# Kernel tuning notes

Measured on AMD Instinct MI355X. Metric: run time of the kernel, lower is better.

## Reference

```python
import jax, jax.numpy as jnp
import numpy as np
import math

FACTOR = 5


def setup_inputs() -> dict:
    key = jax.random.key(0)
    k1, k2, k3, k4 = jax.random.split(key, 4)
    B, L, H, D = 8, 1024, 8, 64
    S = FACTOR * math.ceil(math.log(L))  # U_part = 35
    return {
        "queries": jax.random.normal(k1, (B, L, H, D), jnp.float32),
        "keys": jax.random.normal(k2, (B, L, H, D), jnp.float32),
        "values": jax.random.normal(k3, (B, L, H, D), jnp.float32),
        "sample_idx": jax.random.randint(k4, (L, S), 0, L, dtype=jnp.int32),
        "attn_mask": 0,  # unused by the original forward
    }


def reference(queries, keys, values, sample_idx, attn_mask):
    B, L_Q, H, D = queries.shape
    L_K = keys.shape[1]
    # [B, L, H, D] -> [B, H, L, D]
    Q = jnp.transpose(queries, (0, 2, 1, 3))
    K = jnp.transpose(keys, (0, 2, 1, 3))
    V = jnpp_transpose(values) if False else jnp.transpose(values, (0, 2, 1, 3))

    u = min(FACTOR * math.ceil(math.log(L_Q)), L_Q)  # n_top

    # --- _prob_QK: sampled scores, sparsity measure, top-u query selection ---
    K_sample = K[:, :, sample_idx, :]  # [B, H, L_Q, S, D]
    QK_sample = jnp.einsum('bhqd,bhqsd->bhqs', Q, K_sample)  # [B, H, L_Q, S]
    M = QK_sample.max(axis=-1) - QK_sample.sum(axis=-1) / L_K  # [B, H, L_Q]
    _, M_top = jax.lax.top_k(M, u)  # [B, H, u]

    Q_reduce = jnp.take_along_axis(Q, M_top[..., None], axis=2)  # [B, H, u, D]
    scale = 1.0 / math.sqrt(D)
    scores_top = jnp.einsum('bhud,bhkd->bhuk', Q_reduce, K) * scale  # [B, H, u, L_K]

    # --- initial context (mask_flag=True): running causal mean of V ---
    denom = jnp.arange(1, L_K + 1, dtype=V.dtype)[:, None]  # [L_K, 1]
    context = jnp.cumsum(V, axis=2) / denom  # [B, H, L_K, D]

    # --- softmax over keys, sparse update of selected query rows ---
    attn = jax.nn.softmax(scores_top, axis=-1)  # [B, H, u, L_K]
    update = jnp.einsum('bhuk,bhkd->bhud', attn, V)  # [B, H, u, D]

    b_idx = jnp.arange(B)[:, None, None]
    h_idx = jnp.arange(H)[None, :, None]
    context = context.at[b_idx, h_idx, M_top].set(update)

    return jnp.transpose(context, (0, 2, 1, 3))  # [B, L_Q, H, D]
```

## Files before the change

kernel.cpp:

```cpp
#include <hip/hip_runtime.h>
#include <math.h>

#define BB 8
#define LL 1024
#define HH 8
#define DD 64
#define SS 35
#define UU 35
#define BH (BB*HH)
#define NCHK 4
#define CHK 256
#define RPAD 48

#define CSBLOCKS BH
#define MBLOCKS (BB*LL)

typedef __attribute__((ext_vector_type(8))) short short8;
typedef __attribute__((ext_vector_type(4))) float f32x4;

__device__ __forceinline__ size_t qkv_off(int b, int l, int h, int d) {
    return (((size_t)b*LL + l)*HH + h)*DD + d;
}

__device__ __forceinline__ unsigned short f2bf(float x) {
    unsigned int u = __float_as_uint(x);
    u = (u + 0x7fffu + ((u >> 16) & 1u)) >> 16;
    return (unsigned short)u;
}

__device__ __forceinline__ short8 ld_bf8_g(const float* __restrict__ p) {
    float4 x = *reinterpret_cast<const float4*>(p);
    float4 y = *reinterpret_cast<const float4*>(p + 4);
    short8 r;
    r[0] = (short)f2bf(x.x); r[1] = (short)f2bf(x.y);
    r[2] = (short)f2bf(x.z); r[3] = (short)f2bf(x.w);
    r[4] = (short)f2bf(y.x); r[5] = (short)f2bf(y.y);
    r[6] = (short)f2bf(y.z); r[7] = (short)f2bf(y.w);
    return r;
}

__device__ __forceinline__ float red8_shr(float p) {
    int t;
    t = __builtin_amdgcn_update_dpp(0, __float_as_int(p), 0x111, 0xF, 0xF, true);
    p += __int_as_float(t);
    t = __builtin_amdgcn_update_dpp(0, __float_as_int(p), 0x112, 0xF, 0xF, true);
    p += __int_as_float(t);
    t = __builtin_amdgcn_update_dpp(0, __float_as_int(p), 0x114, 0xF, 0xF, true);
    p += __int_as_float(t);
    return p;
}

__global__ __launch_bounds__(512, 2) void kernel_M_cumsum(const float* __restrict__ Q,
                                                          const float* __restrict__ K,
                                                          const float* __restrict__ V,
                                                          const int*   __restrict__ sidx,
                                                          float* __restrict__ M,
                                                          float* __restrict__ out) {
    int blk = blockIdx.x;
    if (blk < CSBLOCKS) {
        __shared__ float partial[8][64];
        int bh = blk;
        int b = bh >> 3, h = bh & 7;
        int d = threadIdx.x & 63, seg = threadIdx.x >> 6;
        int l0 = seg * 128;
        const float* vp = V + qkv_off(b, l0, h, d);

        float s = 0.f;
#pragma unroll 8
        for (int i = 0; i < 128; i++) s += vp[(size_t)i * (HH * DD)];
        partial[seg][d] = s;
        __syncthreads();
        float run = 0.f;
#pragma unroll
        for (int ss = 0; ss < 7; ss++) {
            float v = partial[ss][d];
            run += (ss < seg) ? v : 0.f;
        }
        float* op = out + qkv_off(b, l0, h, d);
#pragma unroll 8
        for (int i = 0; i < 128; i++) {
            run += vp[(size_t)i * (HH * DD)];
            op[(size_t)i * (HH * DD)] = run / (float)(l0 + i + 1);
        }
    } else {
        __shared__ float s_mx[8][8];
        __shared__ float s_sm[8][8];
        int mblk = blk - CSBLOCKS;
        int b = mblk & 7;
        int q = mblk >> 3;
        int tid = threadIdx.x;
        int w = tid >> 6, lane = tid & 63;
        int h = lane >> 3, j = lane & 7, dsub = j * 4;

        const float* qb = Q + ((size_t)(b * LL + q) * HH + h) * DD + dsub;
        f32x4 q0 = *reinterpret_cast<const f32x4*>(qb);
        f32x4 q1 = *reinterpret_cast<const f32x4*>(qb + 32);

        const int* sq = sidx + q * SS;
        int sl[5];
#pragma unroll
        for (int i = 0; i < 5; i++) {
            int s = w + 8 * i;
            sl[i] = sq[s < SS ? s : 0];
        }

        const float* kbase = K + (size_t)b * (LL * HH * DD) + h * DD + dsub;
        f32x4 ka[5], kc[5];
#pragma unroll
        for (int i = 0; i < 5; i++) {
            const float* kp = kbase + (size_t)sl[i] * (HH * DD);
            ka[i] = *reinterpret_cast<const f32x4*>(kp);
            kc[i] = *reinterpret_cast<const f32x4*>(kp + 32);
        }

        float mx = -INFINITY, sm = 0.f;
#pragma unroll
        for (int i = 0; i < 5; i++) {
            float d = q0.x * ka[i].x + q0.y * ka[i].y + q0.z * ka[i].z + q0.w * ka[i].w
                    + q1.x * kc[i].x + q1.y * kc[i].y + q1.z * kc[i].z + q1.w * kc[i].w;
            d = red8_shr(d);
            bool valid = (i < 4) || (w < 3);
            if (valid) { mx = fmaxf(mx, d); sm += d; }
        }
        if (j == 7) { s_mx[w][h] = mx; s_sm[w][h] = sm; }
        __syncthreads();
        if (tid < 8) {
            float m2 = -INFINITY, s2 = 0.f;
#pragma unroll
            for (int ww = 0; ww < 8; ww++) {
                m2 = fmaxf(m2, s_mx[ww][tid]);
                s2 += s_sm[ww][tid];
            }
            M[(b * HH + tid) * LL + q] = m2 - s2 * (1.0f / LL);
        }
    }
}

__global__ __launch_bounds__(64, 4) void kernel_topk(const float* __restrict__ M,
                                                     int* __restrict__ top) {
    int bh = blockIdx.x, lane = threadIdx.x;
    float v[16];
#pragma unroll
    for (int i = 0; i < 16; i++) v[i] = M[bh * LL + i * 64 + lane];

    for (int k = 0; k < UU; k++) {
        float bv = -INFINITY; int bi = 0x7fffffff;
#pragma unroll
        for (int i = 0; i < 16; i++) {
            if (v[i] > bv) { bv = v[i]; bi = i * 64 + lane; }
        }
#pragma unroll
        for (int w = 1; w < 64; w <<= 1) {
            float ov = __shfl_xor(bv, w);
            int   oi = __shfl_xor(bi, w);
            if (ov > bv || (ov == bv && oi < bi)) { bv = ov; bi = oi; }
        }
        if (lane == 0) top[bh * UU + k] = bi;
        if ((bi & 63) == lane) {
            int slot = bi >> 6;
#pragma unroll
            for (int i = 0; i < 16; i++) if (i == slot) v[i] = -INFINITY;
        }
    }
}

__global__ __launch_bounds__(256) void kernel_attn_part(const float* __restrict__ Q,
                                                        const float* __restrict__ K,
                                                        const float* __restrict__ V,
                                                        const int*   __restrict__ top,
                                                        float* __restrict__ m_ws,
                                                        float* __restrict__ se_ws,
                                                        float* __restrict__ pv_ws) {
    __shared__ unsigned short vt[64 * CHK];
    __shared__ unsigned short p_lds[RPAD * CHK];
    __shared__ float red_m[4][RPAD];
    __shared__ float red_se[4][RPAD];
    __shared__ int   qpos_s[RPAD];

    const int blk = blockIdx.x;
    const int bh  = blk >> 2;
    const int ch  = blk & 3;
    const int b   = bh >> 3, h = bh & 7;
    const int l0  = ch * CHK;
    const int tid = threadIdx.x;
    const int w    = tid >> 6;
    const int lane = tid & 63;
    const int c    = lane & 15;
    const int g    = lane >> 4;
    const float scale = 0.125f;

    if (tid < RPAD) qpos_s[tid] = top[bh * UU + (tid < UU ? tid : UU - 1)];

#pragma unroll
    for (int i = 0; i < 8; i++) {
        int task = i * 256 + tid;
        int d   = task & 63;
        int lq8 = task >> 6;
        float vv[8];
#pragma unroll
        for (int j = 0; j < 8; j++)
            vv[j] = V[qkv_off(b, l0 + lq8 * 8 + j, h, d)];
        short8 pk;
#pragma unroll
        for (int j = 0; j < 8; j++) pk[j] = (short)f2bf(vv[j]);
        *reinterpret_cast<short8*>(vt + d * CHK + (((lq8 ^ (d & 31)) << 3))) = pk;
    }
    __syncthreads();

    f32x4 acc[3][4];
#pragma unroll
    for (int mt = 0; mt < 3; mt++)
#pragma unroll
        for (int nt = 0; nt < 4; nt++) acc[mt][nt] = (f32x4){0.f, 0.f, 0.f, 0.f};

#pragma unroll
    for (int ks = 0; ks < 2; ks++) {
        int k0 = ks * 32 + g * 8;
        short8 af[3];
#pragma unroll
        for (int mt = 0; mt < 3; mt++) {
            int row = mt * 16 + c;
            af[mt] = ld_bf8_g(Q + qkv_off(b, qpos_s[row], h, k0));
        }
#pragma unroll
        for (int nt = 0; nt < 4; nt++) {
            int kl = l0 + w * 64 + nt * 16 + c;
            short8 bf = ld_bf8_g(K + qkv_off(b, kl, h, k0));
#pragma unroll
            for (int mt = 0; mt < 3; mt++)
                acc[mt][nt] = __builtin_amdgcn_mfma_f32_16x16x32_bf16(af[mt], bf, acc[mt][nt], 0, 0, 0);
        }
    }

    float tmax[3][4];
#pragma unroll
    for (int mt = 0; mt < 3; mt++)
#pragma unroll
        for (int r = 0; r < 4; r++) {
            float m = fmaxf(fmaxf(acc[mt][0][r], acc[mt][1][r]),
                            fmaxf(acc[mt][2][r], acc[mt][3][r]));
            m = fmaxf(m, __shfl_xor(m, 1));
            m = fmaxf(m, __shfl_xor(m, 2));
            m = fmaxf(m, __shfl_xor(m, 4));
            m = fmaxf(m, __shfl_xor(m, 8));
            tmax[mt][r] = m;
        }
    if (c == 0) {
#pragma unroll
        for (int mt = 0; mt < 3; mt++)
#pragma unroll
            for (int r = 0; r < 4; r++)
                red_m[w][mt * 16 + g * 4 + r] = tmax[mt][r];
    }
    __syncthreads();

    float tse[3][4];
#pragma unroll
    for (int mt = 0; mt < 3; mt++)
#pragma unroll
        for (int r = 0; r < 4; r++) {
            int row = mt * 16 + g * 4 + r;
            float m = fmaxf(fmaxf(red_m[0][row], red_m[1][row]),
                            fmaxf(red_m[2][row], red_m[3][row]));
            float s = 0.f;
#pragma unroll
            for (int nt = 0; nt < 4; nt++) {
                float p = __expf(scale * (acc[mt][nt][r] - m));
                acc[mt][nt][r] = p;
                s += p;
                p_lds[row * CHK + w * 64 + nt * 16 + c] = f2bf(p);
            }
            s += __shfl_xor(s, 1);
            s += __shfl_xor(s, 2);
            s += __shfl_xor(s, 4);
            s += __shfl_xor(s, 8);
            tse[mt][r] = s;
        }
    if (c == 0) {
#pragma unroll
        for (int mt = 0; mt < 3; mt++)
#pragma unroll
            for (int r = 0; r < 4; r++)
                red_se[w][mt * 16 + g * 4 + r] = tse[mt][r];
    }
    __syncthreads();

    if (tid < RPAD) {
        float mm = fmaxf(fmaxf(red_m[0][tid], red_m[1][tid]),
                         fmaxf(red_m[2][tid], red_m[3][tid]));
        float ss = red_se[0][tid] + red_se[1][tid] + red_se[2][tid] + red_se[3][tid];
        m_ws[blk * RPAD + tid]  = mm;
        se_ws[blk * RPAD + tid] = ss;
    }

    f32x4 acc2[3];
#pragma unroll
    for (int mt = 0; mt < 3; mt++) acc2[mt] = (f32x4){0.f, 0.f, 0.f, 0.f};

#pragma unroll
    for (int ks = 0; ks < 8; ks++) {
        int slot = ks * 4 + g;
        int d    = w * 16 + c;
        short8 bf = *reinterpret_cast<const short8*>(
            vt + d * CHK + ((slot ^ (d & 31)) << 3));
#pragma unroll
        for (int mt = 0; mt < 3; mt++) {
            short8 af = *reinterpret_cast<const short8*>(
                p_lds + (mt * 16 + c) * CHK + ks * 32 + g * 8);
            acc2[mt] = __builtin_amdgcn_mfma_f32_16x16x32_bf16(af, bf, acc2[mt], 0, 0, 0);
        }
    }

#pragma unroll
    for (int mt = 0; mt < 3; mt++)
#pragma unroll
        for (int r = 0; r < 4; r++) {
            int row = mt * 16 + g * 4 + r;
            pv_ws[((size_t)blk * RPAD + row) * 64 + w * 16 + c] = acc2[mt][r];
        }
}

__global__ __launch_bounds__(256) void kernel_attn_comb(const int* __restrict__ top,
                                                        const float* __restrict__ m_ws,
                                                        const float* __restrict__ se_ws,
                                                        const float* __restrict__ pv_ws,
                                                        float* __restrict__ out) {
    int bh = blockIdx.x;
    int b = bh >> 3, h = bh & 7;
    const float scale = 0.125f;
    for (int idx = threadIdx.x; idx < UU * 64; idx += 256) {
        int r = idx >> 6, d = idx & 63;
        float mc[NCHK];
        float mm = -INFINITY;
#pragma unroll
        for (int ch = 0; ch < NCHK; ch++) {
            mc[ch] = m_ws[(bh * NCHK + ch) * RPAD + r];
            mm = fmaxf(mm, mc[ch]);
        }
        float num = 0.f, den = 0.f;
#pragma unroll
        for (int ch = 0; ch < NCHK; ch++) {
            float f = __expf(scale * (mc[ch] - mm));
            num += f * pv_ws[((size_t)(bh * NCHK + ch) * RPAD + r) * 64 + d];
            den += f * se_ws[(bh * NCHK + ch) * RPAD + r];
        }
        out[qkv_off(b, top[bh * UU + r], h, d)] = num / den;
    }
}

extern "C" void kernel_launch(void* const* d_in, const int* in_sizes, int n_in,
                              void* d_out, int out_size, void* d_ws, size_t ws_size,
                              hipStream_t stream) {
    const float* Q    = (const float*)d_in[0];
    const float* K    = (const float*)d_in[1];
    const float* V    = (const float*)d_in[2];
    const int*   sidx = (const int*)d_in[3];
    float* out = (float*)d_out;

    char* ws = (char*)d_ws;
    float* M     = (float*)(ws);
    int*   top   = (int*)  (ws + 262144);
    float* m_ws  = (float*)(ws + 272384);
    float* se_ws = (float*)(ws + 321536);
    float* pv_ws = (float*)(ws + 370688);

    kernel_M_cumsum <<<CSBLOCKS + MBLOCKS, 512, 0, stream>>>(Q, K, V, sidx, M, out);
    kernel_topk     <<<BH, 64, 0, stream>>>(M, top);
    kernel_attn_part<<<BH * NCHK, 256, 0, stream>>>(Q, K, V, top, m_ws, se_ws, pv_ws);
    kernel_attn_comb<<<BH, 256, 0, stream>>>(top, m_ws, se_ws, pv_ws, out);
}
```

Before: 81.59 us.

## Stage sampled K rows via global_load_lds, halve block size, speed topk reduction

```diff
diff --git a/kernel.cpp b/kernel.cpp
--- a/kernel.cpp
+++ b/kernel.cpp
@@ -39,6 +39,12 @@
     return r;
 }
 
+__device__ __forceinline__ void gload_lds16(const void* g, void* l) {
+    __builtin_amdgcn_global_load_lds(
+        (const __attribute__((address_space(1))) void*)g,
+        (__attribute__((address_space(3))) void*)l, 16, 0, 0);
+}
+
 __device__ __forceinline__ float red8_shr(float p) {
     int t;
     t = __builtin_amdgcn_update_dpp(0, __float_as_int(p), 0x111, 0xF, 0xF, true);
@@ -50,7 +56,34 @@
     return p;
 }
 
-__global__ __launch_bounds__(512, 2) void kernel_M_cumsum(const float* __restrict__ Q,
+__device__ __forceinline__ float wave_fmax64(float x) {
+    int t;
+    t = __builtin_amdgcn_update_dpp(0, __float_as_int(x), 0xB1, 0xF, 0xF, true);
+    x = fmaxf(x, __int_as_float(t));
+    t = __builtin_amdgcn_update_dpp(0, __float_as_int(x), 0x4E, 0xF, 0xF, true);
+    x = fmaxf(x, __int_as_float(t));
+    t = __builtin_amdgcn_update_dpp(0, __float_as_int(x), 0x141, 0xF, 0xF, true);
+    x = fmaxf(x, __int_as_float(t));
+    t = __builtin_amdgcn_update_dpp(0, __float_as_int(x), 0x140, 0xF, 0xF, true);
+    x = fmaxf(x, __int_as_float(t));
+    x = fmaxf(x, __shfl_xor(x, 16));
+    x = fmaxf(x, __shfl_xor(x, 32));
+    return x;
+}
+
+__device__ __forceinline__ int wave_imin64(int x) {
+    int t;
+    t = __builtin_amdgcn_update_dpp(0, x, 0xB1, 0xF, 0xF, true);  x = (t < x) ? t : x;
+    t = __builtin_amdgcn_update_dpp(0, x, 0x4E, 0xF, 0xF, true);  x = (t < x) ? t : x;
+    t = __builtin_amdgcn_update_dpp(0, x, 0x141, 0xF, 0xF, true); x = (t < x) ? t : x;
+    t = __builtin_amdgcn_update_dpp(0, x, 0x140, 0xF, 0xF, true); x = (t < x) ? t : x;
+    int y;
+    y = __shfl_xor(x, 16); x = (y < x) ? y : x;
+    y = __shfl_xor(x, 32); x = (y < x) ? y : x;
+    return x;
+}
+
+__global__ __launch_bounds__(256, 3) void kernel_M_cumsum(const float* __restrict__ Q,
                                                           const float* __restrict__ K,
                                                           const float* __restrict__ V,
                                                           const int*   __restrict__ sidx,
@@ -58,76 +91,109 @@
                                                           float* __restrict__ out) {
     int blk = blockIdx.x;
     if (blk < CSBLOCKS) {
-        __shared__ float partial[8][64];
+        __shared__ float partial[4][64];
         int bh = blk;
         int b = bh >> 3, h = bh & 7;
         int d = threadIdx.x & 63, seg = threadIdx.x >> 6;
-        int l0 = seg * 128;
+        int l0 = seg * 256;
         const float* vp = V + qkv_off(b, l0, h, d);
 
         float s = 0.f;
 #pragma unroll 8
-        for (int i = 0; i < 128; i++) s += vp[(size_t)i * (HH * DD)];
+        for (int i = 0; i < 256; i++) s += vp[(size_t)i * (HH * DD)];
         partial[seg][d] = s;
         __syncthreads();
         float run = 0.f;
 #pragma unroll
-        for (int ss = 0; ss < 7; ss++) {
+        for (int ss = 0; ss < 3; ss++) {
             float v = partial[ss][d];
             run += (ss < seg) ? v : 0.f;
         }
         float* op = out + qkv_off(b, l0, h, d);
 #pragma unroll 8
-        for (int i = 0; i < 128; i++) {
+        for (int i = 0; i < 256; i++) {
             run += vp[(size_t)i * (HH * DD)];
             op[(size_t)i * (HH * DD)] = run / (float)(l0 + i + 1);
         }
     } else {
-        __shared__ float s_mx[8][8];
-        __shared__ float s_sm[8][8];
+        __shared__ float rows[4 * 2560];
+        __shared__ float s_mx[4][8];
+        __shared__ float s_sm[4][8];
         int mblk = blk - CSBLOCKS;
         int b = mblk & 7;
         int q = mblk >> 3;
         int tid = threadIdx.x;
         int w = tid >> 6, lane = tid & 63;
-        int h = lane >> 3, j = lane & 7, dsub = j * 4;
-
-        const float* qb = Q + ((size_t)(b * LL + q) * HH + h) * DD + dsub;
+        int h = lane >> 3, j = lane & 7;
+
+        const float* qb = Q + ((size_t)(b * LL + q) * HH + h) * DD + j * 4;
         f32x4 q0 = *reinterpret_cast<const f32x4*>(qb);
         f32x4 q1 = *reinterpret_cast<const f32x4*>(qb + 32);
 
-        const int* sq = sidx + q * SS;
-        int sl[5];
-#pragma unroll
-        for (int i = 0; i < 5; i++) {
-            int s = w + 8 * i;
-            sl[i] = sq[s < SS ? s : 0];
-        }
-
-        const float* kbase = K + (size_t)b * (LL * HH * DD) + h * DD + dsub;
-        f32x4 ka[5], kc[5];
-#pragma unroll
-        for (int i = 0; i < 5; i++) {
-            const float* kp = kbase + (size_t)sl[i] * (HH * DD);
-            ka[i] = *reinterpret_cast<const f32x4*>(kp);
-            kc[i] = *reinterpret_cast<const f32x4*>(kp + 32);
-        }
+        const int* sq = sidx + q * SS + w * 9;
+        const char* kb = (const char*)(K + (size_t)b * (LL * HH * DD));
+        char* region = (char*)(rows + w * 2560);
+        const float* region_f = rows + w * 2560;
 
         float mx = -INFINITY, sm = 0.f;
-#pragma unroll
-        for (int i = 0; i < 5; i++) {
-            float d = q0.x * ka[i].x + q0.y * ka[i].y + q0.z * ka[i].z + q0.w * ka[i].w
-                    + q1.x * kc[i].x + q1.y * kc[i].y + q1.z * kc[i].z + q1.w * kc[i].w;
-            d = red8_shr(d);
-            bool valid = (i < 4) || (w < 3);
-            if (valid) { mx = fmaxf(mx, d); sm += d; }
-        }
+
+        {
+            int sl[5];
+#pragma unroll
+            for (int i = 0; i < 5; i++) sl[i] = sq[i];
+#pragma unroll
+            for (int r = 0; r < 5; r++) {
+                const char* gsrc = kb + (size_t)sl[r] * 2048 + lane * 16;
+                gload_lds16(gsrc,        region + r * 2048);
+                gload_lds16(gsrc + 1024, region + r * 2048 + 1024);
+            }
+            asm volatile("s_waitcnt vmcnt(0)" ::: "memory");
+#pragma unroll
+            for (int r = 0; r < 5; r++) {
+                const float* rp = region_f + r * 512 + h * 64 + j * 4;
+                f32x4 k0 = *reinterpret_cast<const f32x4*>(rp);
+                f32x4 k1 = *reinterpret_cast<const f32x4*>(rp + 32);
+                float d = q0.x * k0.x + q0.y * k0.y + q0.z * k0.z + q0.w * k0.w
+                        + q1.x * k1.x + q1.y * k1.y + q1.z * k1.z + q1.w * k1.w;
+                d = red8_shr(d);
+                mx = fmaxf(mx, d); sm += d;
+            }
+            asm volatile("s_waitcnt lgkmcnt(0)" ::: "memory");
+        }
+
+        {
+            int sl[4];
+#pragma unroll
+            for (int i = 0; i < 4; i++) {
+                int ii = (i == 3 && w == 3) ? 2 : i;
+                sl[i] = sq[5 + ii];
+            }
+#pragma unroll
+            for (int r = 0; r < 4; r++) {
+                const char* gsrc = kb + (size_t)sl[r] * 2048 + lane * 16;
+                gload_lds16(gsrc,        region + r * 2048);
+                gload_lds16(gsrc + 1024, region + r * 2048 + 1024);
+            }
+            asm volatile("s_waitcnt vmcnt(0)" ::: "memory");
+#pragma unroll
+            for (int r = 0; r < 4; r++) {
+                const float* rp = region_f + r * 512 + h * 64 + j * 4;
+                f32x4 k0 = *reinterpret_cast<const f32x4*>(rp);
+                f32x4 k1 = *reinterpret_cast<const f32x4*>(rp + 32);
+                float d = q0.x * k0.x + q0.y * k0.y + q0.z * k0.z + q0.w * k0.w
+                        + q1.x * k1.x + q1.y * k1.y + q1.z * k1.z + q1.w * k1.w;
+                d = red8_shr(d);
+                bool valid = (r < 3) || (w < 3);
+                if (valid) { mx = fmaxf(mx, d); sm += d; }
+            }
+        }
+
         if (j == 7) { s_mx[w][h] = mx; s_sm[w][h] = sm; }
         __syncthreads();
         if (tid < 8) {
             float m2 = -INFINITY, s2 = 0.f;
 #pragma unroll
-            for (int ww = 0; ww < 8; ww++) {
+            for (int ww = 0; ww < 4; ww++) {
                 m2 = fmaxf(m2, s_mx[ww][tid]);
                 s2 += s_sm[ww][tid];
             }
@@ -144,20 +210,17 @@
     for (int i = 0; i < 16; i++) v[i] = M[bh * LL + i * 64 + lane];
 
     for (int k = 0; k < UU; k++) {
-        float bv = -INFINITY; int bi = 0x7fffffff;
+        float bv = -INFINITY; int bslot = 0;
 #pragma unroll
         for (int i = 0; i < 16; i++) {
-            if (v[i] > bv) { bv = v[i]; bi = i * 64 + lane; }
-        }
-#pragma unroll
-        for (int w = 1; w < 64; w <<= 1) {
-            float ov = __shfl_xor(bv, w);
-            int   oi = __shfl_xor(bi, w);
-            if (ov > bv || (ov == bv && oi < bi)) { bv = ov; bi = oi; }
-        }
-        if (lane == 0) top[bh * UU + k] = bi;
-        if ((bi & 63) == lane) {
-            int slot = bi >> 6;
+            if (v[i] > bv) { bv = v[i]; bslot = i; }
+        }
+        float wm = wave_fmax64(bv);
+        int gidx = (bv == wm) ? (bslot * 64 + lane) : 0x7fffffff;
+        int widx = wave_imin64(gidx);
+        if (lane == 0) top[bh * UU + k] = widx;
+        if ((widx & 63) == lane) {
+            int slot = widx >> 6;
 #pragma unroll
             for (int i = 0; i < 16; i++) if (i == slot) v[i] = -INFINITY;
         }
@@ -198,11 +261,11 @@
         int lq8 = task >> 6;
         float vv[8];
 #pragma unroll
-        for (int j = 0; j < 8; j++)
-            vv[j] = V[qkv_off(b, l0 + lq8 * 8 + j, h, d)];
+        for (int jj = 0; jj < 8; jj++)
+            vv[jj] = V[qkv_off(b, l0 + lq8 * 8 + jj, h, d)];
         short8 pk;
 #pragma unroll
-        for (int j = 0; j < 8; j++) pk[j] = (short)f2bf(vv[j]);
+        for (int jj = 0; jj < 8; jj++) pk[jj] = (short)f2bf(vv[jj]);
         *reinterpret_cast<short8*>(vt + d * CHK + (((lq8 ^ (d & 31)) << 3))) = pk;
     }
     __syncthreads();
@@ -364,7 +427,7 @@
     float* se_ws = (float*)(ws + 321536);
     float* pv_ws = (float*)(ws + 370688);
 
-    kernel_M_cumsum <<<CSBLOCKS + MBLOCKS, 512, 0, stream>>>(Q, K, V, sidx, M, out);
+    kernel_M_cumsum <<<CSBLOCKS + MBLOCKS, 256, 0, stream>>>(Q, K, V, sidx, M, out);
     kernel_topk     <<<BH, 64, 0, stream>>>(M, top);
     kernel_attn_part<<<BH * NCHK, 256, 0, stream>>>(Q, K, V, top, m_ws, se_ws, pv_ws);
     kernel_attn_comb<<<BH, 256, 0, stream>>>(top, m_ws, se_ws, pv_ws, out);
```

Measured after the change: 75.93 us. 6.9% less time.
